# Kernel optimization log

Hardware: AMD Instinct MI355X
Metric: run time of the kernel (lower is better)

Reference implementation:

```python
import jax, jax.numpy as jnp
import numpy as np

NEG_SLOPE = 0.01  # torch LeakyReLU default

def leaky_relu(x):
    return jnp.where(x >= 0, x, NEG_SLOPE * x)

def gcn_conv(h, W, b, src, dst, n):
    # PyG GCNConv: linear (no bias), add self-loops, symmetric norm, scatter-add, + bias
    h = h @ W  # [N, F]
    loop = jnp.arange(n, dtype=src.dtype)
    s = jnp.concatenate([src, loop])
    d = jnp.concatenate([dst, loop])
    deg = jax.ops.segment_sum(jnp.ones_like(d, dtype=h.dtype), d, num_segments=n)
    dinv = jnp.where(deg > 0, deg ** -0.5, 0.0)
    norm = dinv[s] * dinv[d]  # [E+N]
    msg = h[s] * norm[:, None]
    out = jax.ops.segment_sum(msg, d, num_segments=n)
    return out + b

def setup_inputs() -> dict:
    key = jax.random.key(0)
    ks = jax.random.split(key, 12)
    N, E, D_IN, D_H, D_OUT, C = 100000, 3200000, 512, 128, 64, 2
    def lin(k, fi, fo):
        bound = 1.0 / np.sqrt(fi)
        k1, k2 = jax.random.split(k)
        W = jax.random.uniform(k1, (fi, fo), jnp.float32, -bound, bound)
        b = jax.random.uniform(k2, (fo,), jnp.float32, -bound, bound)
        return W, b
    W1, b1 = lin(ks[0], D_IN, D_H)
    W2, b2 = lin(ks[1], D_H, D_OUT)
    Wg1, bg1 = lin(ks[2], D_OUT, D_OUT)
    Wg2, bg2 = lin(ks[3], D_OUT, D_OUT)
    Wc, bc = lin(ks[4], D_OUT, C)
    x = jax.random.normal(ks[5], (N, D_IN), jnp.float32)
    edge_index = jax.random.randint(ks[6], (2, E), 0, N, jnp.int32)
    return {"x": x, "edge_index": edge_index, "W1": W1, "b1": b1, "W2": W2, "b2": b2,
            "Wg1": Wg1, "bg1": bg1, "Wg2": Wg2, "bg2": bg2, "Wc": Wc, "bc": bc}

def reference(x, edge_index, W1, b1, W2, b2, Wg1, bg1, Wg2, bg2, Wc, bc):
    n = x.shape[0]
    src, dst = edge_index[0], edge_index[1]
    # encoder (dropout = identity in eval)
    h = leaky_relu(x @ W1 + b1)
    h = leaky_relu(h @ W2 + b2)
    # two GCN layers
    h = leaky_relu(gcn_conv(h, Wg1, bg1, src, dst, n))
    h = leaky_relu(gcn_conv(h, Wg2, bg2, src, dst, n))
    logits = h @ Wc + bc
    return logits, h
```

## Files before the change

kernel.cpp:

```cpp
#include <hip/hip_runtime.h>
#include <hip/hip_bf16.h>

typedef __bf16 v8bf16 __attribute__((ext_vector_type(8)));
typedef float  v4f32  __attribute__((ext_vector_type(4)));
typedef unsigned short ushort8v __attribute__((ext_vector_type(8)));

static __device__ __forceinline__ float leaky(float v) { return v >= 0.0f ? v : 0.01f * v; }
static __device__ __forceinline__ float bfbits2f(unsigned short b) {
    union { unsigned u; float f; } c; c.u = ((unsigned)b) << 16; return c.f;
}
static __device__ __forceinline__ unsigned short f2bfbits(float f) {
    __hip_bfloat16 h = __float2bfloat16(f);
    unsigned short s; __builtin_memcpy(&s, &h, 2); return s;
}

constexpr int EPB  = 6400;
constexpr int BCAP = 16384;

static __device__ __forceinline__ bool role_split(int bid, int nA, int tot,
                                                  int& idxA, int& idxB) {
    const long long s0 = (long long)bid * nA / tot;
    const long long s1 = (long long)(bid + 1) * nA / tot;
    if (s1 > s0) { idxA = (int)s0; idxB = 0; return true; }
    idxA = 0; idxB = bid - (int)s0; return false;
}

__global__ __launch_bounds__(256) void prep_all(
    const float* __restrict__ W1, const float* __restrict__ W2,
    const float* __restrict__ Wg1,
    __hip_bfloat16* __restrict__ W1f, __hip_bfloat16* __restrict__ W2t,
    __hip_bfloat16* __restrict__ Wg1t,
    unsigned* __restrict__ bcur, int DIN, int DH, int DO, int NB) {
    const int fragTotal  = DIN * DH;
    const int fragBlocks = (fragTotal + 255) / 256;
    const int n2 = DH * DO, ng = DO * DO;
    const int smallTotal  = n2 + ng;
    const int smallBlocks = (smallTotal + 255) / 256;
    const int bid = blockIdx.x;
    if (bid < fragBlocks) {
        int tid = bid * 256 + threadIdx.x;
        if (tid >= fragTotal) return;
        int j = tid & 7, l = (tid >> 3) & 63, G = tid >> 9;
        int m = l & 15, q = l >> 4;
        int t = G & 7, kk = G >> 3;
        int n = t * 16 + m;
        int k = kk * 32 + q * 8 + j;
        W1f[tid] = __float2bfloat16(W1[k * DH + n]);
    } else if (bid < fragBlocks + smallBlocks) {
        int i = (bid - fragBlocks) * 256 + threadIdx.x;
        if (i < n2) {
            int r = i / DO, c = i % DO;
            W2t[c * DH + r] = __float2bfloat16(W2[i]);
        } else if (i < smallTotal) {
            int j = i - n2; int r = j / DO, c = j % DO;
            Wg1t[c * DO + r] = __float2bfloat16(Wg1[j]);
        }
    } else {
        int i = (bid - fragBlocks - smallBlocks) * 256 + threadIdx.x;
        if (i < NB) bcur[i] = 0u;
    }
}

struct ScatterSmem {
    unsigned stg[EPB];
    unsigned hist[512], inc[512], cur[512], start[512];
};

static __device__ __forceinline__ void scatter_body(
    int bid, ScatterSmem& sm, const int* __restrict__ src, const int* __restrict__ dst,
    unsigned* __restrict__ bcur, unsigned* __restrict__ ebuck, int E, int NB) {
    const int tid = threadIdx.x;
    sm.hist[tid] = 0u;
    __syncthreads();
    const int beg = bid * EPB;
    const int end = min(beg + EPB, E);
    unsigned myd[13];
#pragma unroll
    for (int i = 0; i < 13; i++) {
        const int e = beg + tid + i * 512;
        if (e < end) {
            const unsigned d = (unsigned)dst[e];
            myd[i] = d;
            atomicAdd(&sm.hist[d >> 8], 1u);
        }
    }
    __syncthreads();
    const unsigned h = sm.hist[tid];
    sm.inc[tid] = h;
    __syncthreads();
    for (int off = 1; off < 512; off <<= 1) {
        unsigned t = (tid >= off) ? sm.inc[tid - off] : 0u;
        __syncthreads();
        sm.inc[tid] += t;
        __syncthreads();
    }
    sm.cur[tid] = sm.inc[tid] - h;
    if (tid < NB && h > 0u)
        sm.start[tid] = (unsigned)tid * BCAP + atomicAdd(&bcur[tid], h);
    __syncthreads();
#pragma unroll
    for (int i = 0; i < 13; i++) {
        const int e = beg + tid + i * 512;
        if (e < end) {
            const unsigned b = myd[i] >> 8;
            const unsigned r = atomicAdd(&sm.cur[b], 1u);
            sm.stg[r] = (unsigned)e;
        }
    }
    __syncthreads();
    const int cnt = end - beg;
    for (int s = tid; s < cnt; s += 512) {
        const unsigned e = sm.stg[s];
        const unsigned d = (unsigned)dst[e];
        const unsigned b = d >> 8;
        const unsigned excl = sm.inc[b] - sm.hist[b];
        const unsigned pos = sm.start[b] + ((unsigned)s - excl);
        ebuck[pos] = (unsigned)src[e] | ((d & 255u) << 20);
    }
}

static __device__ __forceinline__ void enc1_body(
    int bid, uint4 (*lds)[1024], const float* __restrict__ A, const uint4* __restrict__ Bp,
    const float* __restrict__ bias, __hip_bfloat16* __restrict__ C, int M) {
    constexpr int K = 512;
    const int tid = threadIdx.x;
    const int wid = tid >> 6, lane = tid & 63;
    const int m = lane & 15, q = lane >> 4;
    const int row0 = bid * 128 + wid * 16;
    const int rowA = row0 + m;
    const int rowAc = rowA < M ? rowA : M - 1;
    const float* Ap = A + (size_t)rowAc * K + q * 8;

    v4f32 acc[8];
#pragma unroll
    for (int t = 0; t < 8; t++) acc[t] = (v4f32){0.f, 0.f, 0.f, 0.f};

    float4 ab[2][4];

    auto loadA = [&](int c, int par) {
#pragma unroll
        for (int j = 0; j < 4; j++)
            ab[par][j] = *reinterpret_cast<const float4*>(Ap + c * 64 + (j >> 1) * 32 + (j & 1) * 4);
    };
    auto stage = [&](int c, int par) {
        lds[par][tid]       = Bp[c * 1024 + tid];
        lds[par][512 + tid] = Bp[c * 1024 + 512 + tid];
    };

    stage(0, 0);
    loadA(0, 0);
    for (int c = 0; c < 8; c++) {
        __syncthreads();
        if (c < 7) { stage(c + 1, (c + 1) & 1); loadA(c + 1, (c + 1) & 1); }
        const int par = c & 1;
#pragma unroll
        for (int kk2 = 0; kk2 < 2; kk2++) {
            float4 f0 = ab[par][kk2 * 2], f1 = ab[par][kk2 * 2 + 1];
            v8bf16 a = {(__bf16)f0.x, (__bf16)f0.y, (__bf16)f0.z, (__bf16)f0.w,
                        (__bf16)f1.x, (__bf16)f1.y, (__bf16)f1.z, (__bf16)f1.w};
#pragma unroll
            for (int t = 0; t < 8; t++) {
                v8bf16 b = reinterpret_cast<const v8bf16*>(lds[par])[(kk2 * 8 + t) * 64 + lane];
                acc[t] = __builtin_amdgcn_mfma_f32_16x16x32_bf16(a, b, acc[t], 0, 0, 0);
            }
        }
    }

#pragma unroll
    for (int r = 0; r < 4; r++) {
        const int row = row0 + q * 4 + r;
        if (row >= M) continue;
#pragma unroll
        for (int t = 0; t < 8; t++) {
            const int col = t * 16 + m;
            C[(size_t)row * 128 + col] = __float2bfloat16(leaky(acc[t][r] + bias[col]));
        }
    }
}

__global__ __launch_bounds__(512, 4) void mega_scatter_enc1(
    const int* __restrict__ src, const int* __restrict__ dst,
    unsigned* __restrict__ bcur, unsigned* __restrict__ ebuck, int E, int NB, int nScatter,
    const float* __restrict__ A, const uint4* __restrict__ Bp,
    const float* __restrict__ bias, __hip_bfloat16* __restrict__ C, int M) {
    union Smem {
        ScatterSmem sc;
        uint4 g[2][1024];
    };
    __shared__ Smem sm;
    int ia, ib;
    if (role_split(blockIdx.x, nScatter, gridDim.x, ia, ib))
        scatter_body(ia, sm.sc, src, dst, bcur, ebuck, E, NB);
    else
        enc1_body(ib, sm.g, A, Bp, bias, C, M);
}

template <int NT, int MODE>
static __device__ __forceinline__ void gemm_body(
    int bid, const __hip_bfloat16* __restrict__ A, const __hip_bfloat16* __restrict__ Bt,
    const float* __restrict__ bias, const float* __restrict__ dinv,
    __hip_bfloat16* __restrict__ Cbf, int M, int K) {
    const int wid  = threadIdx.x >> 6;
    const int lane = threadIdx.x & 63;
    const int row0 = (bid * 4 + wid) << 4;
    if (row0 >= M) return;
    const int m = lane & 15, q = lane >> 4;

    const __hip_bfloat16* Ab = A + (size_t)(row0 + m) * K + q * 8;

    v4f32 acc[NT];
#pragma unroll
    for (int t = 0; t < NT; t++) acc[t] = (v4f32){0.f, 0.f, 0.f, 0.f};

    for (int k0 = 0; k0 < K; k0 += 32) {
        v8bf16 a = *reinterpret_cast<const v8bf16*>(Ab + k0);
#pragma unroll
        for (int t = 0; t < NT; t++) {
            v8bf16 b = *reinterpret_cast<const v8bf16*>(Bt + (size_t)(t * 16 + m) * K + k0 + q * 8);
            acc[t] = __builtin_amdgcn_mfma_f32_16x16x32_bf16(a, b, acc[t], 0, 0, 0);
        }
    }

    const int N = NT * 16;
#pragma unroll
    for (int r = 0; r < 4; r++) {
        const int row = row0 + q * 4 + r;
        float di = (MODE == 1) ? dinv[row] : 1.0f;
#pragma unroll
        for (int t = 0; t < NT; t++) {
            const int col = t * 16 + m;
            float v = acc[t][r];
            if (MODE == 0) v = leaky(v + bias[col]);
            else           v *= di;
            Cbf[(size_t)row * N + col] = __float2bfloat16(v);
        }
    }
}

template <int NT, int MODE>
__global__ __launch_bounds__(256) void gemm_kernel(
    const __hip_bfloat16* __restrict__ A, const __hip_bfloat16* __restrict__ Bt,
    const float* __restrict__ bias, const float* __restrict__ dinv,
    __hip_bfloat16* __restrict__ Cbf, int M, int K) {
    gemm_body<NT, MODE>(blockIdx.x, A, Bt, bias, dinv, Cbf, M, K);
}

static __device__ __forceinline__ void csr_body(
    int k, unsigned* hist, unsigned* cur, const unsigned* __restrict__ bcur,
    const unsigned* __restrict__ ebuck, uint2* __restrict__ rp2,
    float* __restrict__ dinv, int* __restrict__ csr, int NN) {
    const int tid = threadIdx.x;
    const unsigned cntb = bcur[k];
    const unsigned base = (unsigned)k * BCAP;
    const unsigned* eb = ebuck + base;
    hist[tid] = 0u;
    __syncthreads();
    for (unsigned e = tid; e < cntb; e += 256)
        atomicAdd(&hist[eb[e] >> 20], 1u);
    __syncthreads();
    const unsigned h = hist[tid];
    cur[tid] = h;
    __syncthreads();
    for (int off = 1; off < 256; off <<= 1) {
        unsigned t = (tid >= off) ? cur[tid - off] : 0u;
        __syncthreads();
        cur[tid] += t;
        __syncthreads();
    }
    const unsigned excl = cur[tid] - h;
    const int node = k * 256 + tid;
    if (node < NN) {
        rp2[node] = make_uint2(base + excl, base + excl + h);
        dinv[node] = rsqrtf((float)(h + 1u));
    }
    __syncthreads();
    cur[tid] = excl;
    __syncthreads();
    for (unsigned e = tid; e < cntb; e += 256) {
        const unsigned pk = eb[e];
        const unsigned pos = base + atomicAdd(&cur[pk >> 20], 1u);
        csr[pos] = (int)(pk & 0xFFFFFu);
    }
}

__global__ __launch_bounds__(256) void mega_csr_enc2(
    const unsigned* __restrict__ bcur, const unsigned* __restrict__ ebuck,
    uint2* __restrict__ rp2, float* __restrict__ dinv, int* __restrict__ csr,
    int NN, int nCsr,
    const __hip_bfloat16* __restrict__ A, const __hip_bfloat16* __restrict__ Bt,
    const float* __restrict__ bias, __hip_bfloat16* __restrict__ Cb, int M, int K) {
    __shared__ unsigned hist[256], cur[256];
    int ia, ib;
    if (role_split(blockIdx.x, nCsr, gridDim.x, ia, ib))
        csr_body(ia, hist, cur, bcur, ebuck, rp2, dinv, csr, NN);
    else
        gemm_body<4, 0>(ib, A, Bt, bias, nullptr, Cb, M, K);
}

template <int HEAD>
__global__ __launch_bounds__(256) void gather_kernel(
    const uint2* __restrict__ rp2, const int* __restrict__ csr_src,
    const __hip_bfloat16* __restrict__ u, const float* __restrict__ dinv,
    const float* __restrict__ bias, __hip_bfloat16* __restrict__ out_bf,
    float* __restrict__ out_h, const float* __restrict__ Wmid,
    const float* __restrict__ bc, float* __restrict__ out_logits, int n) {
    const int node = blockIdx.x * 4 + (threadIdx.x >> 6);
    if (node >= n) return;
    const int lane = threadIdx.x & 63;
    const int g = lane >> 3, t = lane & 7;
    const uint2 rp = rp2[node];
    const unsigned beg = rp.x, end = rp.y;

    float s[8];
#pragma unroll
    for (int j = 0; j < 8; j++) s[j] = 0.f;

    unsigned e = beg + g;
    bool hA = e < end, hB = e + 8 < end;
    int sA = hA ? csr_src[e] : 0;
    int sB = hB ? csr_src[e + 8] : 0;
    while (hA) {
        const unsigned en = e + 16;
        const bool hA2 = en < end, hB2 = en + 8 < end;
        const int sA2 = hA2 ? csr_src[en] : 0;
        const int sB2 = hB2 ? csr_src[en + 8] : 0;
        ushort8v wA = *reinterpret_cast<const ushort8v*>(u + (size_t)sA * 64 + t * 8);
        if (hB) {
            ushort8v wB = *reinterpret_cast<const ushort8v*>(u + (size_t)sB * 64 + t * 8);
#pragma unroll
            for (int j = 0; j < 8; j++) s[j] += bfbits2f(wA[j]) + bfbits2f(wB[j]);
        } else {
#pragma unroll
            for (int j = 0; j < 8; j++) s[j] += bfbits2f(wA[j]);
        }
        e = en; hA = hA2; hB = hB2; sA = sA2; sB = sB2;
    }
#pragma unroll
    for (int j = 0; j < 8; j++) {
        s[j] += __shfl_xor(s[j], 8, 64);
        s[j] += __shfl_xor(s[j], 16, 64);
        s[j] += __shfl_xor(s[j], 32, 64);
    }

    ushort8v wsr = *reinterpret_cast<const ushort8v*>(u + (size_t)node * 64 + t * 8);
#pragma unroll
    for (int j = 0; j < 8; j++) s[j] += bfbits2f(wsr[j]);

    const float di = dinv[node];
    const float4 b0 = *reinterpret_cast<const float4*>(bias + t * 8);
    const float4 b1 = *reinterpret_cast<const float4*>(bias + t * 8 + 4);
    float f[8];
    f[0] = leaky(s[0] * di + b0.x); f[1] = leaky(s[1] * di + b0.y);
    f[2] = leaky(s[2] * di + b0.z); f[3] = leaky(s[3] * di + b0.w);
    f[4] = leaky(s[4] * di + b1.x); f[5] = leaky(s[5] * di + b1.y);
    f[6] = leaky(s[6] * di + b1.z); f[7] = leaky(s[7] * di + b1.w);

    if (HEAD == 0) {
        float a0 = 0.f, a1 = 0.f;
#pragma unroll
        for (int j = 0; j < 64; j += 2) {
            const float r0 = __shfl(f[j & 7], j >> 3, 64);
            const float r1 = __shfl(f[(j + 1) & 7], (j + 1) >> 3, 64);
            a0 += r0 * Wmid[j * 64 + lane];
            a1 += r1 * Wmid[(j + 1) * 64 + lane];
        }
        out_bf[(size_t)node * 64 + lane] = __float2bfloat16((a0 + a1) * di);
    } else {
        if (g == 0) {
            float4 o0 = {f[0], f[1], f[2], f[3]};
            float4 o1 = {f[4], f[5], f[6], f[7]};
            *reinterpret_cast<float4*>(out_h + (size_t)node * 64 + t * 8) = o0;
            *reinterpret_cast<float4*>(out_h + (size_t)node * 64 + t * 8 + 4) = o1;
        }
        float p0 = 0.f, p1 = 0.f;
#pragma unroll
        for (int j = 0; j < 8; j++) {
            p0 += f[j] * Wmid[(t * 8 + j) * 2];
            p1 += f[j] * Wmid[(t * 8 + j) * 2 + 1];
        }
#pragma unroll
        for (int o = 4; o; o >>= 1) {
            p0 += __shfl_xor(p0, o, 64);
            p1 += __shfl_xor(p1, o, 64);
        }
        if (lane == 0) {
            out_logits[(size_t)node * 2 + 0] = p0 + bc[0];
            out_logits[(size_t)node * 2 + 1] = p1 + bc[1];
        }
    }
}

extern "C" void kernel_launch(void* const* d_in, const int* in_sizes, int n_in,
                              void* d_out, int out_size, void* d_ws, size_t ws_size,
                              hipStream_t stream) {
    const float* x   = (const float*)d_in[0];
    const int*   ei  = (const int*)d_in[1];
    const float* W1  = (const float*)d_in[2];
    const float* b1  = (const float*)d_in[3];
    const float* W2  = (const float*)d_in[4];
    const float* b2  = (const float*)d_in[5];
    const float* Wg1 = (const float*)d_in[6];
    const float* bg1 = (const float*)d_in[7];
    const float* Wg2 = (const float*)d_in[8];
    const float* bg2 = (const float*)d_in[9];
    const float* Wc  = (const float*)d_in[10];
    const float* bc  = (const float*)d_in[11];

    const int DH  = in_sizes[3];
    const int DIN = in_sizes[2] / DH;
    const int NN  = in_sizes[0] / DIN;
    const int E   = in_sizes[1] / 2;
    const int DO  = in_sizes[5];
    const int* src = ei;
    const int* dst = ei + E;

    char*  ws  = (char*)d_ws;
    size_t off = 0;
    auto alloc = [&](size_t bytes) {
        void* p = ws + off;
        off += (bytes + 255) & ~(size_t)255;
        return p;
    };
    const int NB = (NN + 255) >> 8;
    __hip_bfloat16* h1    = (__hip_bfloat16*)alloc((size_t)NN * DH * 2);
    __hip_bfloat16* h2    = (__hip_bfloat16*)alloc((size_t)NN * DO * 2);
    __hip_bfloat16* ub    = (__hip_bfloat16*)alloc((size_t)NN * DO * 2);
    __hip_bfloat16* ub2   = (__hip_bfloat16*)alloc((size_t)NN * DO * 2);
    float*          dinv  = (float*)alloc((size_t)NN * 4);
    uint2*          rp2   = (uint2*)alloc((size_t)NN * 8);
    int*            csr   = (int*)alloc((size_t)NB * BCAP * 4);
    unsigned*       ebuck = (unsigned*)alloc((size_t)NB * BCAP * 4);
    unsigned*       bcur  = (unsigned*)alloc(512 * 4);
    __hip_bfloat16* W1f   = (__hip_bfloat16*)alloc((size_t)DIN * DH * 2);
    __hip_bfloat16* W2t   = (__hip_bfloat16*)alloc((size_t)DH * DO * 2);
    __hip_bfloat16* Wg1t  = (__hip_bfloat16*)alloc((size_t)DO * DO * 2);

    float* out_logits = (float*)d_out;
    float* out_h      = (float*)d_out + (size_t)NN * 2;

    const int fragBlocks  = (DIN * DH + 255) / 256;
    const int smallBlocks = (DH * DO + DO * DO + 255) / 256;
    const int zeroBlocks  = (NB + 255) / 256;
    prep_all<<<fragBlocks + smallBlocks + zeroBlocks, 256, 0, stream>>>(
        W1, W2, Wg1, W1f, W2t, Wg1t, bcur, DIN, DH, DO, NB);

    const int nblkP = (E + EPB - 1) / EPB;
    const int enc1B = (NN + 127) / 128;
    mega_scatter_enc1<<<nblkP + enc1B, 512, 0, stream>>>(
        src, dst, bcur, ebuck, E, NB, nblkP,
        x, (const uint4*)W1f, b1, h1, NN);

    const int gemm_blocks = (NN / 16 + 3) / 4;
    mega_csr_enc2<<<NB + gemm_blocks, 256, 0, stream>>>(
        bcur, ebuck, rp2, dinv, csr, NN, NB,
        h1, W2t, b2, h2, NN, DH);

    gemm_kernel<4, 1><<<gemm_blocks, 256, 0, stream>>>(h2, Wg1t, nullptr, dinv, ub, NN, DO);
    gather_kernel<0><<<(NN + 3) / 4, 256, 0, stream>>>(rp2, csr, ub, dinv, bg1, ub2,
                                                       nullptr, Wg2, nullptr, nullptr, NN);
    gather_kernel<1><<<(NN + 3) / 4, 256, 0, stream>>>(rp2, csr, ub2, dinv, bg2, nullptr,
                                                       out_h, Wc, bc, out_logits, NN);
}
```

Before: 580.9 us.

## Move second GCN linear into MFMA gemm and read enc1 weights directly

The second GCN layer's 64x64 linear was a per-node shuffle-based FMA loop inside the first gather kernel. It now runs as a separate MFMA gemm_kernel launch on a bf16-transposed Wg2 produced in prep_all, and the gather writes leaky-relu features straight to bf16. The encoder-1 body also drops its LDS double-buffered staging of W1 fragments and barriers, loading B fragments from global/L2 each iteration. This adds one kernel launch and an extra NxD round trip through memory, in exchange for cheaper gather work and fewer syncs.

```diff
diff --git a/kernel.cpp b/kernel.cpp
--- a/kernel.cpp
+++ b/kernel.cpp
@@ -27,14 +27,14 @@
 
 __global__ __launch_bounds__(256) void prep_all(
     const float* __restrict__ W1, const float* __restrict__ W2,
-    const float* __restrict__ Wg1,
+    const float* __restrict__ Wg1, const float* __restrict__ Wg2,
     __hip_bfloat16* __restrict__ W1f, __hip_bfloat16* __restrict__ W2t,
-    __hip_bfloat16* __restrict__ Wg1t,
+    __hip_bfloat16* __restrict__ Wg1t, __hip_bfloat16* __restrict__ Wg2t,
     unsigned* __restrict__ bcur, int DIN, int DH, int DO, int NB) {
     const int fragTotal  = DIN * DH;
     const int fragBlocks = (fragTotal + 255) / 256;
     const int n2 = DH * DO, ng = DO * DO;
-    const int smallTotal  = n2 + ng;
+    const int smallTotal  = n2 + 2 * ng;
     const int smallBlocks = (smallTotal + 255) / 256;
     const int bid = blockIdx.x;
     if (bid < fragBlocks) {
@@ -51,9 +51,12 @@
         if (i < n2) {
             int r = i / DO, c = i % DO;
             W2t[c * DH + r] = __float2bfloat16(W2[i]);
-        } else if (i < smallTotal) {
+        } else if (i < n2 + ng) {
             int j = i - n2; int r = j / DO, c = j % DO;
             Wg1t[c * DO + r] = __float2bfloat16(Wg1[j]);
+        } else if (i < smallTotal) {
+            int j = i - n2 - ng; int r = j / DO, c = j % DO;
+            Wg2t[c * DO + r] = __float2bfloat16(Wg2[j]);
         }
     } else {
         int i = (bid - fragBlocks - smallBlocks) * 256 + threadIdx.x;
@@ -120,7 +123,7 @@
 }
 
 static __device__ __forceinline__ void enc1_body(
-    int bid, uint4 (*lds)[1024], const float* __restrict__ A, const uint4* __restrict__ Bp,
+    int bid, const float* __restrict__ A, const v8bf16* __restrict__ Bp,
     const float* __restrict__ bias, __hip_bfloat16* __restrict__ C, int M) {
     constexpr int K = 512;
     const int tid = threadIdx.x;
@@ -136,22 +139,16 @@
     for (int t = 0; t < 8; t++) acc[t] = (v4f32){0.f, 0.f, 0.f, 0.f};
 
     float4 ab[2][4];
-
     auto loadA = [&](int c, int par) {
 #pragma unroll
         for (int j = 0; j < 4; j++)
             ab[par][j] = *reinterpret_cast<const float4*>(Ap + c * 64 + (j >> 1) * 32 + (j & 1) * 4);
     };
-    auto stage = [&](int c, int par) {
-        lds[par][tid]       = Bp[c * 1024 + tid];
-        lds[par][512 + tid] = Bp[c * 1024 + 512 + tid];
-    };
-
-    stage(0, 0);
+
     loadA(0, 0);
+#pragma unroll
     for (int c = 0; c < 8; c++) {
-        __syncthreads();
-        if (c < 7) { stage(c + 1, (c + 1) & 1); loadA(c + 1, (c + 1) & 1); }
+        if (c < 7) loadA(c + 1, (c + 1) & 1);
         const int par = c & 1;
 #pragma unroll
         for (int kk2 = 0; kk2 < 2; kk2++) {
@@ -160,7 +157,7 @@
                         (__bf16)f1.x, (__bf16)f1.y, (__bf16)f1.z, (__bf16)f1.w};
 #pragma unroll
             for (int t = 0; t < 8; t++) {
-                v8bf16 b = reinterpret_cast<const v8bf16*>(lds[par])[(kk2 * 8 + t) * 64 + lane];
+                v8bf16 b = Bp[(size_t)(c * 16 + kk2 * 8 + t) * 64 + lane];
                 acc[t] = __builtin_amdgcn_mfma_f32_16x16x32_bf16(a, b, acc[t], 0, 0, 0);
             }
         }
@@ -181,18 +178,14 @@
 __global__ __launch_bounds__(512, 4) void mega_scatter_enc1(
     const int* __restrict__ src, const int* __restrict__ dst,
     unsigned* __restrict__ bcur, unsigned* __restrict__ ebuck, int E, int NB, int nScatter,
-    const float* __restrict__ A, const uint4* __restrict__ Bp,
+    const float* __restrict__ A, const v8bf16* __restrict__ Bp,
     const float* __restrict__ bias, __hip_bfloat16* __restrict__ C, int M) {
-    union Smem {
-        ScatterSmem sc;
-        uint4 g[2][1024];
-    };
-    __shared__ Smem sm;
+    __shared__ ScatterSmem sm;
     int ia, ib;
     if (role_split(blockIdx.x, nScatter, gridDim.x, ia, ib))
-        scatter_body(ia, sm.sc, src, dst, bcur, ebuck, E, NB);
+        scatter_body(ia, sm, src, dst, bcur, ebuck, E, NB);
     else
-        enc1_body(ib, sm.g, A, Bp, bias, C, M);
+        enc1_body(ib, A, Bp, bias, C, M);
 }
 
 template <int NT, int MODE>
@@ -302,7 +295,7 @@
     const uint2* __restrict__ rp2, const int* __restrict__ csr_src,
     const __hip_bfloat16* __restrict__ u, const float* __restrict__ dinv,
     const float* __restrict__ bias, __hip_bfloat16* __restrict__ out_bf,
-    float* __restrict__ out_h, const float* __restrict__ Wmid,
+    float* __restrict__ out_h, const float* __restrict__ Wc,
     const float* __restrict__ bc, float* __restrict__ out_logits, int n) {
     const int node = blockIdx.x * 4 + (threadIdx.x >> 6);
     if (node >= n) return;
@@ -356,15 +349,12 @@
     f[6] = leaky(s[6] * di + b1.z); f[7] = leaky(s[7] * di + b1.w);
 
     if (HEAD == 0) {
-        float a0 = 0.f, a1 = 0.f;
-#pragma unroll
-        for (int j = 0; j < 64; j += 2) {
-            const float r0 = __shfl(f[j & 7], j >> 3, 64);
-            const float r1 = __shfl(f[(j + 1) & 7], (j + 1) >> 3, 64);
-            a0 += r0 * Wmid[j * 64 + lane];
-            a1 += r1 * Wmid[(j + 1) * 64 + lane];
-        }
-        out_bf[(size_t)node * 64 + lane] = __float2bfloat16((a0 + a1) * di);
+        if (g == 0) {
+            ushort8v o;
+#pragma unroll
+            for (int j = 0; j < 8; j++) o[j] = f2bfbits(f[j]);
+            *reinterpret_cast<ushort8v*>(out_bf + (size_t)node * 64 + t * 8) = o;
+        }
     } else {
         if (g == 0) {
             float4 o0 = {f[0], f[1], f[2], f[3]};
@@ -375,8 +365,8 @@
         float p0 = 0.f, p1 = 0.f;
 #pragma unroll
         for (int j = 0; j < 8; j++) {
-            p0 += f[j] * Wmid[(t * 8 + j) * 2];
-            p1 += f[j] * Wmid[(t * 8 + j) * 2 + 1];
+            p0 += f[j] * Wc[(t * 8 + j) * 2];
+            p1 += f[j] * Wc[(t * 8 + j) * 2 + 1];
         }
 #pragma unroll
         for (int o = 4; o; o >>= 1) {
@@ -424,8 +414,8 @@
     const int NB = (NN + 255) >> 8;
     __hip_bfloat16* h1    = (__hip_bfloat16*)alloc((size_t)NN * DH * 2);
     __hip_bfloat16* h2    = (__hip_bfloat16*)alloc((size_t)NN * DO * 2);
+    __hip_bfloat16* h3    = (__hip_bfloat16*)alloc((size_t)NN * DO * 2);
     __hip_bfloat16* ub    = (__hip_bfloat16*)alloc((size_t)NN * DO * 2);
-    __hip_bfloat16* ub2   = (__hip_bfloat16*)alloc((size_t)NN * DO * 2);
     float*          dinv  = (float*)alloc((size_t)NN * 4);
     uint2*          rp2   = (uint2*)alloc((size_t)NN * 8);
     int*            csr   = (int*)alloc((size_t)NB * BCAP * 4);
@@ -434,21 +424,22 @@
     __hip_bfloat16* W1f   = (__hip_bfloat16*)alloc((size_t)DIN * DH * 2);
     __hip_bfloat16* W2t   = (__hip_bfloat16*)alloc((size_t)DH * DO * 2);
     __hip_bfloat16* Wg1t  = (__hip_bfloat16*)alloc((size_t)DO * DO * 2);
+    __hip_bfloat16* Wg2t  = (__hip_bfloat16*)alloc((size_t)DO * DO * 2);
 
     float* out_logits = (float*)d_out;
     float* out_h      = (float*)d_out + (size_t)NN * 2;
 
     const int fragBlocks  = (DIN * DH + 255) / 256;
-    const int smallBlocks = (DH * DO + DO * DO + 255) / 256;
+    const int smallBlocks = (DH * DO + 2 * DO * DO + 255) / 256;
     const int zeroBlocks  = (NB + 255) / 256;
     prep_all<<<fragBlocks + smallBlocks + zeroBlocks, 256, 0, stream>>>(
-        W1, W2, Wg1, W1f, W2t, Wg1t, bcur, DIN, DH, DO, NB);
+        W1, W2, Wg1, Wg2, W1f, W2t, Wg1t, Wg2t, bcur, DIN, DH, DO, NB);
 
     const int nblkP = (E + EPB - 1) / EPB;
     const int enc1B = (NN + 127) / 128;
     mega_scatter_enc1<<<nblkP + enc1B, 512, 0, stream>>>(
         src, dst, bcur, ebuck, E, NB, nblkP,
-        x, (const uint4*)W1f, b1, h1, NN);
+        x, (const v8bf16*)W1f, b1, h1, NN);
 
     const int gemm_blocks = (NN / 16 + 3) / 4;
     mega_csr_enc2<<<NB + gemm_blocks, 256, 0, stream>>>(
@@ -456,8 +447,10 @@
         h1, W2t, b2, h2, NN, DH);
 
     gemm_kernel<4, 1><<<gemm_blocks, 256, 0, stream>>>(h2, Wg1t, nullptr, dinv, ub, NN, DO);
-    gather_kernel<0><<<(NN + 3) / 4, 256, 0, stream>>>(rp2, csr, ub, dinv, bg1, ub2,
-                                                       nullptr, Wg2, nullptr, nullptr, NN);
-    gather_kernel<1><<<(NN + 3) / 4, 256, 0, stream>>>(rp2, csr, ub2, dinv, bg2, nullptr,
+    gather_kernel<0><<<(NN + 3) / 4, 256, 0, stream>>>(rp2, csr, ub, dinv, bg1, h3,
+                                                       nullptr, nullptr, nullptr, nullptr, NN);
+
+    gemm_kernel<4, 1><<<gemm_blocks, 256, 0, stream>>>(h3, Wg2t, nullptr, dinv, ub, NN, DO);
+    gather_kernel<1><<<(NN + 3) / 4, 256, 0, stream>>>(rp2, csr, ub, dinv, bg2, nullptr,
                                                        out_h, Wc, bc, out_logits, NN);
 }
```

Result: slower. 596.5 us (+2.7%).
